# Optimization experiments

Measured on AMD Instinct MI355X. Metric: run time of the kernel, lower is better.

## Reference

```python
import jax, jax.numpy as jnp
import numpy as np

B, IN, H = 8192, 1024, 1024
WRANK, UR0, UR1, G = 256, 64, 32, 2
HG = H // G


def setup_inputs() -> dict:
    key = jax.random.key(0)
    ks = jax.random.split(key, 24)
    r = lambda k, shp: 0.1 * jax.random.normal(k, shp, dtype=jnp.float32)
    inp = {
        "x": jax.random.normal(ks[0], (B, IN), dtype=jnp.float32),
        "h": jax.random.normal(ks[1], (B, H), dtype=jnp.float32),
        "c": jax.random.normal(ks[2], (B, H), dtype=jnp.float32),
        "W": r(ks[3], (IN, WRANK)),
        "W1": r(ks[4], (WRANK, H)),
        "W2": r(ks[5], (WRANK, H)),
        "W3": r(ks[6], (WRANK, H)),
        "W4": r(ks[7], (WRANK, H)),
        "U": r(ks[8], (G, HG, UR0)),
        "U1": r(ks[9], (G, UR0, HG)),
        "U2": r(ks[10], (G, UR0, HG)),
        "U3": r(ks[11], (G, UR0, HG)),
        "U4": r(ks[12], (G, UR0, HG)),
        "UU": r(ks[13], (G, HG, UR1)),
        "UU1": r(ks[14], (G, UR1, HG)),
        "UU2": r(ks[15], (G, UR1, HG)),
        "UU3": r(ks[16], (G, UR1, HG)),
        "UU4": r(ks[17], (G, UR1, HG)),
        "bias_f": jnp.ones((1, H), dtype=jnp.float32),
        "bias_i": jnp.ones((1, H), dtype=jnp.float32),
        "bias_c": jnp.ones((1, H), dtype=jnp.float32),
        "bias_o": jnp.ones((1, H), dtype=jnp.float32),
    }
    return inp


def _grouped(hg, Ushare, Ui):
    # hg: [B, g, hg]; Ushare: [g, hg, r]; Ui: [g, r, hg] -> [B, H]
    t = jnp.einsum('bgd,gdr->bgr', hg, Ushare)
    return jnp.einsum('bgr,grd->bgd', t, Ui).reshape(hg.shape[0], H)


def reference(x, h, c, W, W1, W2, W3, W4, U, U1, U2, U3, U4,
              UU, UU1, UU2, UU3, UU4, bias_f, bias_i, bias_c, bias_o):
    # low-rank W path
    xw = x @ W                      # [B, wRank]
    wVal1, wVal2, wVal3, wVal4 = xw @ W1, xw @ W2, xw @ W3, xw @ W4

    # grouped low-rank U path (diagonal groups)
    hg = h.reshape(B, G, HG)
    tU = jnp.einsum('bgd,gdr->bgr', hg, U)          # shared projection
    uVal1 = jnp.einsum('bgr,grd->bgd', tU, U1).reshape(B, H)
    uVal2 = jnp.einsum('bgr,grd->bgd', tU, U2).reshape(B, H)
    uVal3 = jnp.einsum('bgr,grd->bgd', tU, U3).reshape(B, H)
    uVal4 = jnp.einsum('bgr,grd->bgd', tU, U4).reshape(B, H)

    # grouped UU path on group-rotated h (index = [1..g-1, 0])
    hg3 = jnp.roll(hg, -1, axis=1)
    tUU = jnp.einsum('bgd,gdr->bgr', hg3, UU)
    uuVal1 = jnp.einsum('bgr,grd->bgd', tUU, UU1).reshape(B, H)
    uuVal2 = jnp.einsum('bgr,grd->bgd', tUU, UU2).reshape(B, H)
    uuVal3 = jnp.einsum('bgr,grd->bgd', tUU, UU3).reshape(B, H)
    uuVal4 = jnp.einsum('bgr,grd->bgd', tUU, UU4).reshape(B, H)

    matVal_i = wVal1 + uVal1 + uuVal1
    matVal_f = wVal2 + uVal2 + uuVal2
    matVal_o = wVal3 + uVal3 + uuVal3
    matVal_c = wVal4 + uVal4 + uuVal4

    i = jax.nn.sigmoid(matVal_i + bias_i)
    f = jax.nn.sigmoid(matVal_f + bias_f)
    o = jax.nn.sigmoid(matVal_o + bias_o)
    c_tilda = jnp.tanh(matVal_c + bias_c)

    c_next = f * c + i * c_tilda
    h_next = o * jnp.tanh(c_next)
    return (c_next, h_next)
```

## Files before the change

### kernel.cpp

```cpp
#include <hip/hip_runtime.h>
#include <hip/hip_bf16.h>

#define B_ROWS 8192
#define IN_DIM 1024
#define H_DIM  1024
#define WRANK  256
#define UR0    64
#define UR1    32
#define HGD    512

#define NS2    11
#define NTA    14

typedef __attribute__((ext_vector_type(8))) short bf16x8;
typedef __attribute__((ext_vector_type(4))) float f32x4;
typedef __attribute__((ext_vector_type(4))) float float4v;

__device__ __forceinline__ unsigned short f2bf(float f) {
    union { float f; unsigned u; } v; v.f = f;
    unsigned r = v.u + 0x7FFF + ((v.u >> 16) & 1);
    return (unsigned short)(r >> 16);
}

__device__ __forceinline__ void gld16(void* lds, const void* g) {
    __builtin_amdgcn_global_load_lds(
        (const __attribute__((address_space(1))) unsigned int*)g,
        (__attribute__((address_space(3))) unsigned int*)lds, 16, 0, 0);
}

__device__ __forceinline__ float fsig(float x)  { return 1.f / (1.f + __expf(-x)); }
__device__ __forceinline__ float ftanh(float x) { return 1.f - 2.f / (__expf(2.f * x) + 1.f); }

__global__ __launch_bounds__(256)
void pack_weights(const float* __restrict__ W,
                  const float* __restrict__ W1, const float* __restrict__ W2,
                  const float* __restrict__ W3, const float* __restrict__ W4,
                  const float* __restrict__ U,  const float* __restrict__ U1,
                  const float* __restrict__ U2, const float* __restrict__ U3,
                  const float* __restrict__ U4,
                  const float* __restrict__ UU, const float* __restrict__ UU1,
                  const float* __restrict__ UU2,const float* __restrict__ UU3,
                  const float* __restrict__ UU4,
                  unsigned short* __restrict__ WbfT,
                  unsigned short* __restrict__ HPbf,
                  unsigned short* __restrict__ BT2)
{
    const float* Wg[4]  = {W1, W2, W3, W4};
    const float* Ug[4]  = {U1, U2, U3, U4};
    const float* UUg[4] = {UU1, UU2, UU3, UU4};
    const long N_WT = 256L * 1024;
    const long N_HP = 256L * 512;
    const long N_BT = 16L * NS2 * 8192;
    const long total = N_WT + N_HP + N_BT;
    for (long t = blockIdx.x * 256L + threadIdx.x; t < total; t += (long)gridDim.x * 256L) {
        if (t < N_WT) {
            int n = (int)(t >> 10), p = (int)(t & 1023);
            int span = p >> 6, slp = (p >> 3) & 7, e = p & 7;
            int k = span * 64 + ((slp ^ (n & 7)) << 3) + e;
            WbfT[t] = f2bf(W[(size_t)k * WRANK + n]);
        } else if (t < N_WT + N_HP) {
            long u = t - N_WT;
            int n = (int)(u >> 9), p = (int)(u & 511);
            int span = p >> 6, slp = (p >> 3) & 7, e = p & 7;
            int k = span * 64 + ((slp ^ (n & 7)) << 3) + e;
            float v;
            if (n < 64)       v = U [(size_t)k * UR0 + n];
            else if (n < 96)  v = UU[(size_t)(HGD + k) * UR1 + (n - 64)];
            else if (n < 128) v = 0.f;
            else if (n < 192) v = U [(size_t)(HGD + k) * UR0 + (n - 128)];
            else if (n < 224) v = UU[(size_t)k * UR1 + (n - 192)];
            else              v = 0.f;
            HPbf[u] = f2bf(v);
        } else {
            long u = t - N_WT - N_HP;
            int img = (int)(u >> 13);
            int nt = img / NS2, s = img % NS2;
            int r = (int)(u & 8191);
            int q = r >> 11, kc = (r >> 9) & 3, row = (r >> 3) & 63, e = r & 7;
            int n = nt * 64 + row, g = n >> 9, nn = n & 511;
            int kk = kc * 8 + e;
            float v;
            if (s < 8)       v = Wg[q][(size_t)(s * 32 + kk) * H_DIM + n];
            else if (s < 10) v = Ug[q][((size_t)g * UR0 + (s - 8) * 32 + kk) * HGD + nn];
            else             v = UUg[q][((size_t)g * UR1 + kk) * HGD + nn];
            BT2[u] = f2bf(v);
        }
    }
}

__global__ __launch_bounds__(256, 4)
void s1_kernel(const float* __restrict__ x, const float* __restrict__ h,
               const unsigned short* __restrict__ WbfT,
               const unsigned short* __restrict__ HPbf,
               unsigned short* __restrict__ A2T)
{
    __shared__ short As[64 * 64];
    __shared__ short Bs[2][64 * 64];

    const int flat = blockIdx.x;
    const int id = (flat & 7) * 128 + (flat >> 3);
    const int bx = id & 7, by = id >> 3;
    const int m0 = by * 64;

    const bool pa = bx < 4;
    const int Kdim = pa ? IN_DIM : HGD;
    const float* Af = pa ? x : h;
    const int a_off = pa ? 0 : ((bx - 4) >> 1) * HGD;
    const unsigned short* Bw = pa ? (WbfT + (size_t)(bx * 64) * IN_DIM)
                                  : (HPbf + (size_t)((bx - 4) * 64) * HGD);
    const int ldbw = pa ? IN_DIM : HGD;
    const int ccol0 = pa ? bx * 64 : WRANK + (bx - 4) * 64;

    const int tid = threadIdx.x, lane = tid & 63, wid = tid >> 6;
    const int wr = wid >> 1, wc = wid & 1;
    const int lr = lane & 15, lh = lane >> 4;
    const int l8 = lane >> 3, l7 = lane & 7;

    f32x4 acc[2][2];
    #pragma unroll
    for (int i = 0; i < 2; ++i)
        #pragma unroll
        for (int j = 0; j < 2; ++j) acc[i][j] = (f32x4){0.f, 0.f, 0.f, 0.f};

    float4v areg[2][2][2];

#define S1_STAGEB(buf, kk) do {                                                   \
    _Pragma("unroll")                                                             \
    for (int t = 0; t < 2; ++t) {                                                 \
        int u = wid * 2 + t;                                                      \
        gld16((char*)&Bs[buf][0] + u * 1024,                                      \
              (const char*)Bw + ((size_t)(u * 8 + l8) * ldbw + (kk)) * 2 + l7 * 16); \
    } } while (0)

#define S1_LOADA(set, kk) do {                                                    \
    _Pragma("unroll")                                                             \
    for (int t = 0; t < 2; ++t) {                                                 \
        int cc = tid + t * 256;                                                   \
        int row = cc >> 3, slot = cc & 7;                                         \
        const float* p = Af + (size_t)(m0 + row) * 1024 + a_off + (kk) + slot * 8;\
        areg[set][t][0] = *(const float4v*)p;                                     \
        areg[set][t][1] = *(const float4v*)(p + 4);                               \
    } } while (0)

#define S1_WRITEA(set) do {                                                       \
    _Pragma("unroll")                                                             \
    for (int t = 0; t < 2; ++t) {                                                 \
        int cc = tid + t * 256;                                                   \
        int row = cc >> 3, slot = cc & 7;                                         \
        union { bf16x8 v; unsigned short s_[8]; } uv;                             \
        uv.s_[0] = f2bf(areg[set][t][0].x); uv.s_[1] = f2bf(areg[set][t][0].y);   \
        uv.s_[2] = f2bf(areg[set][t][0].z); uv.s_[3] = f2bf(areg[set][t][0].w);   \
        uv.s_[4] = f2bf(areg[set][t][1].x); uv.s_[5] = f2bf(areg[set][t][1].y);   \
        uv.s_[6] = f2bf(areg[set][t][1].z); uv.s_[7] = f2bf(areg[set][t][1].w);   \
        *(bf16x8*)((char*)As + row * 128 + ((slot ^ (row & 7)) << 4)) = uv.v;     \
    } } while (0)

    S1_STAGEB(0, 0);
    S1_LOADA(0, 0);

    #pragma unroll
    for (int ki = 0; ki < 16; ++ki) {
        if (ki * 64 >= Kdim) break;
        const int cur = ki & 1;
        const bool more = (ki + 1) * 64 < Kdim;
        if (more) S1_STAGEB(cur ^ 1, (ki + 1) * 64);
        if (more) { asm volatile("s_waitcnt vmcnt(2)" ::: "memory"); }
        else      { asm volatile("s_waitcnt vmcnt(0)" ::: "memory"); }
        S1_WRITEA(cur);
        if (more) S1_LOADA(cur ^ 1, (ki + 1) * 64);
        asm volatile("s_waitcnt lgkmcnt(0)" ::: "memory");
        __builtin_amdgcn_s_barrier();
        asm volatile("" ::: "memory");
        #pragma unroll
        for (int ks = 0; ks < 2; ++ks) {
            bf16x8 af[2];
            #pragma unroll
            for (int i = 0; i < 2; ++i) {
                int r = wr * 32 + i * 16 + lr;
                af[i] = *(const bf16x8*)((const char*)As + r * 128
                        + (((ks * 4 + lh) ^ (r & 7)) << 4));
            }
            #pragma unroll
            for (int j = 0; j < 2; ++j) {
                int r = wc * 32 + j * 16 + lr;
                bf16x8 rb = *(const bf16x8*)((const char*)&Bs[cur][0] + r * 128
                            + (((ks * 4 + lh) ^ (r & 7)) << 4));
                #pragma unroll
                for (int i = 0; i < 2; ++i)
                    acc[i][j] = __builtin_amdgcn_mfma_f32_16x16x32_bf16(
                        af[i], rb, acc[i][j], 0, 0, 0);
            }
        }
        asm volatile("" ::: "memory");
        __builtin_amdgcn_s_barrier();
        asm volatile("" ::: "memory");
    }
#undef S1_STAGEB
#undef S1_LOADA
#undef S1_WRITEA

    #pragma unroll
    for (int i = 0; i < 2; ++i) {
        #pragma unroll
        for (int j = 0; j < 2; ++j) {
            int ncol = ccol0 + wc * 32 + j * 16 + lr;
            int blk = ncol >> 5;
            if (blk == 11 || blk == 15) continue;
            int tt = (blk <= 10) ? blk : blk - 1;
            int kk = ncol & 31, kc = kk >> 3, e = kk & 7;
            #pragma unroll
            for (int rr = 0; rr < 4; ++rr) {
                int brow = m0 + wr * 32 + i * 16 + lh * 4 + rr;
                A2T[((size_t)(brow >> 8) * NTA + tt) * 8192 + kc * 2048
                    + (brow & 255) * 8 + e] = f2bf(acc[i][j][rr]);
            }
        }
    }
}

__global__ __launch_bounds__(512, 4)
void s2_kernel(const unsigned short* __restrict__ A2T,
               const unsigned short* __restrict__ BT2,
               const float* __restrict__ bias_f, const float* __restrict__ bias_i,
               const float* __restrict__ bias_c, const float* __restrict__ bias_o,
               const float* __restrict__ cin,
               float* __restrict__ cout, float* __restrict__ hout)
{
    __shared__ short As[3][4 * 128 * 8];
    __shared__ short Bs[3][4 * 4 * 64 * 8];

    const int flat = blockIdx.x;
    const int id = (flat & 7) * 128 + (flat >> 3);
    const int nt = id & 15, mt = id >> 4;
    const int m0 = mt * 128, n0 = nt * 64, g = nt >> 3;

    const int tid = threadIdx.x, lane = tid & 63, wid = tid >> 6;
    const int wr = wid >> 2, wc = wid & 3;
    const int lr = lane & 15, lh = lane >> 4;

    const char* Abase = (const char*)A2T + (size_t)(mt >> 1) * NTA * 16384
                        + (wid >> 1) * 4096 + (mt & 1) * 2048 + (wid & 1) * 1024
                        + lane * 16;
    const char* Bbase = (const char*)BT2 + (size_t)nt * NS2 * 16384 + lane * 16;

    f32x4 acc[4][4];
    #pragma unroll
    for (int q = 0; q < 4; ++q)
        #pragma unroll
        for (int i = 0; i < 4; ++i) acc[q][i] = (f32x4){0.f, 0.f, 0.f, 0.f};

#define S2_TA(s) ((s) < 8 ? (s) : (g == 0 ? ((s) == 10 ? 13 : (s)) \
                                          : ((s) == 10 ? 10 : (s) + 3)))
#define S2_STAGE(buf, s, tA) do {                                                 \
    gld16((char*)&As[buf][0] + wid * 1024, Abase + (size_t)(tA) * 16384);         \
    _Pragma("unroll")                                                             \
    for (int t = 0; t < 2; ++t) {                                                 \
        int v = wid * 2 + t;                                                      \
        gld16((char*)&Bs[buf][0] + v * 1024,                                      \
              Bbase + (size_t)(s) * 16384 + v * 1024);                            \
    } } while (0)

    S2_STAGE(0, 0, 0);
    S2_STAGE(1, 1, 1);

    #pragma unroll
    for (int s = 0; s < NS2; ++s) {
        const int cur = s % 3;
        if (s + 2 < NS2) {
            S2_STAGE((s + 2) % 3, s + 2, S2_TA(s + 2));
            asm volatile("s_waitcnt vmcnt(6)" ::: "memory");
        } else if (s + 1 < NS2) {
            asm volatile("s_waitcnt vmcnt(3)" ::: "memory");
        } else {
            asm volatile("s_waitcnt vmcnt(0)" ::: "memory");
        }
        __builtin_amdgcn_s_barrier();
        asm volatile("" ::: "memory");

        bf16x8 rb[4];
        #pragma unroll
        for (int q = 0; q < 4; ++q)
            rb[q] = *(const bf16x8*)((const char*)&Bs[cur][0]
                    + q * 4096 + lh * 1024 + (wc * 16 + lr) * 16);
        {
            bf16x8 af0 = *(const bf16x8*)((const char*)&As[cur][0]
                         + lh * 2048 + (wr * 64 + 0 * 16 + lr) * 16);
            bf16x8 af1 = *(const bf16x8*)((const char*)&As[cur][0]
                         + lh * 2048 + (wr * 64 + 1 * 16 + lr) * 16);
            __builtin_amdgcn_s_setprio(1);
            #pragma unroll
            for (int q = 0; q < 4; ++q) {
                acc[q][0] = __builtin_amdgcn_mfma_f32_16x16x32_bf16(af0, rb[q], acc[q][0], 0, 0, 0);
                acc[q][1] = __builtin_amdgcn_mfma_f32_16x16x32_bf16(af1, rb[q], acc[q][1], 0, 0, 0);
            }
            __builtin_amdgcn_s_setprio(0);
        }
        asm volatile("" ::: "memory");
        __builtin_amdgcn_s_barrier();
        asm volatile("" ::: "memory");

        {
            bf16x8 af2 = *(const bf16x8*)((const char*)&As[cur][0]
                         + lh * 2048 + (wr * 64 + 2 * 16 + lr) * 16);
            bf16x8 af3 = *(const bf16x8*)((const char*)&As[cur][0]
                         + lh * 2048 + (wr * 64 + 3 * 16 + lr) * 16);
            __builtin_amdgcn_s_setprio(1);
            #pragma unroll
            for (int q = 0; q < 4; ++q) {
                acc[q][2] = __builtin_amdgcn_mfma_f32_16x16x32_bf16(af2, rb[q], acc[q][2], 0, 0, 0);
                acc[q][3] = __builtin_amdgcn_mfma_f32_16x16x32_bf16(af3, rb[q], acc[q][3], 0, 0, 0);
            }
            __builtin_amdgcn_s_setprio(0);
        }
        asm volatile("" ::: "memory");
        __builtin_amdgcn_s_barrier();
        asm volatile("" ::: "memory");
    }
#undef S2_STAGE
#undef S2_TA

    const int ncol = n0 + wc * 16 + lr;
    const float Bi = bias_i[ncol], Bf = bias_f[ncol];
    const float Bo = bias_o[ncol], Bc = bias_c[ncol];
    #pragma unroll
    for (int i = 0; i < 4; ++i) {
        #pragma unroll
        for (int rr = 0; rr < 4; ++rr) {
            int brow = m0 + wr * 64 + i * 16 + lh * 4 + rr;
            float mi = acc[0][i][rr] + Bi;
            float mf = acc[1][i][rr] + Bf;
            float mo = acc[2][i][rr] + Bo;
            float mc = acc[3][i][rr] + Bc;
            float iv = fsig(mi), fv = fsig(mf), ov = fsig(mo);
            float ct = ftanh(mc);
            float cv = cin[(size_t)brow * H_DIM + ncol];
            float cn = fv * cv + iv * ct;
            float hn = ov * ftanh(cn);
            cout[(size_t)brow * H_DIM + ncol] = cn;
            hout[(size_t)brow * H_DIM + ncol] = hn;
        }
    }
}

extern "C" void kernel_launch(void* const* d_in, const int* in_sizes, int n_in,
                              void* d_out, int out_size, void* d_ws, size_t ws_size,
                              hipStream_t stream)
{
    const float* x   = (const float*)d_in[0];
    const float* h   = (const float*)d_in[1];
    const float* c   = (const float*)d_in[2];
    const float* W   = (const float*)d_in[3];
    const float* W1  = (const float*)d_in[4];
    const float* W2  = (const float*)d_in[5];
    const float* W3  = (const float*)d_in[6];
    const float* W4  = (const float*)d_in[7];
    const float* U   = (const float*)d_in[8];
    const float* U1  = (const float*)d_in[9];
    const float* U2  = (const float*)d_in[10];
    const float* U3  = (const float*)d_in[11];
    const float* U4  = (const float*)d_in[12];
    const float* UU  = (const float*)d_in[13];
    const float* UU1 = (const float*)d_in[14];
    const float* UU2 = (const float*)d_in[15];
    const float* UU3 = (const float*)d_in[16];
    const float* UU4 = (const float*)d_in[17];
    const float* bias_f = (const float*)d_in[18];
    const float* bias_i = (const float*)d_in[19];
    const float* bias_c = (const float*)d_in[20];
    const float* bias_o = (const float*)d_in[21];

    unsigned short* A2T  = (unsigned short*)d_ws;
    unsigned short* WbfT = A2T  + 32L * NTA * 8192;
    unsigned short* HPbf = WbfT + 256L * 1024;
    unsigned short* BT2  = HPbf + 256L * 512;

    float* c_out = (float*)d_out;
    float* h_out = c_out + (size_t)B_ROWS * H_DIM;

    pack_weights<<<dim3(2048), dim3(256), 0, stream>>>(
        W, W1, W2, W3, W4, U, U1, U2, U3, U4, UU, UU1, UU2, UU3, UU4,
        WbfT, HPbf, BT2);

    s1_kernel<<<dim3(1024), dim3(256), 0, stream>>>(x, h, WbfT, HPbf, A2T);

    s2_kernel<<<dim3(1024), dim3(512), 0, stream>>>(
        A2T, BT2, bias_f, bias_i, bias_c, bias_o, c, c_out, h_out);
}
```

Baseline: 83.15 us.

## Move second-stage weight packing into extra s1 blocks to overlap with GEMM

The BT2 weight packing (W1-4, U1-4, UU1-4 to bf16 tiles) moves out of pack_weights and into 512 extra blocks appended to the s1 launch, so it runs concurrently with the first-stage GEMM. pack_weights now only packs the s1 operands with fewer blocks. This shortens the serial pre-pass but adds branch and argument overhead to s1, and the packing blocks compete with the GEMM for CUs and bandwidth.

```diff
diff --git a/kernel.cpp b/kernel.cpp
--- a/kernel.cpp
+++ b/kernel.cpp
@@ -33,32 +33,20 @@
 
 __global__ __launch_bounds__(256)
 void pack_weights(const float* __restrict__ W,
-                  const float* __restrict__ W1, const float* __restrict__ W2,
-                  const float* __restrict__ W3, const float* __restrict__ W4,
-                  const float* __restrict__ U,  const float* __restrict__ U1,
-                  const float* __restrict__ U2, const float* __restrict__ U3,
-                  const float* __restrict__ U4,
-                  const float* __restrict__ UU, const float* __restrict__ UU1,
-                  const float* __restrict__ UU2,const float* __restrict__ UU3,
-                  const float* __restrict__ UU4,
+                  const float* __restrict__ U,  const float* __restrict__ UU,
                   unsigned short* __restrict__ WbfT,
-                  unsigned short* __restrict__ HPbf,
-                  unsigned short* __restrict__ BT2)
+                  unsigned short* __restrict__ HPbf)
 {
-    const float* Wg[4]  = {W1, W2, W3, W4};
-    const float* Ug[4]  = {U1, U2, U3, U4};
-    const float* UUg[4] = {UU1, UU2, UU3, UU4};
     const long N_WT = 256L * 1024;
     const long N_HP = 256L * 512;
-    const long N_BT = 16L * NS2 * 8192;
-    const long total = N_WT + N_HP + N_BT;
+    const long total = N_WT + N_HP;
     for (long t = blockIdx.x * 256L + threadIdx.x; t < total; t += (long)gridDim.x * 256L) {
         if (t < N_WT) {
             int n = (int)(t >> 10), p = (int)(t & 1023);
             int span = p >> 6, slp = (p >> 3) & 7, e = p & 7;
             int k = span * 64 + ((slp ^ (n & 7)) << 3) + e;
             WbfT[t] = f2bf(W[(size_t)k * WRANK + n]);
-        } else if (t < N_WT + N_HP) {
+        } else {
             long u = t - N_WT;
             int n = (int)(u >> 9), p = (int)(u & 511);
             int span = p >> 6, slp = (p >> 3) & 7, e = p & 7;
@@ -71,8 +59,33 @@
             else if (n < 224) v = UU[(size_t)k * UR1 + (n - 192)];
             else              v = 0.f;
             HPbf[u] = f2bf(v);
-        } else {
-            long u = t - N_WT - N_HP;
+        }
+    }
+}
+
+__global__ __launch_bounds__(256, 4)
+void s1_kernel(const float* __restrict__ x, const float* __restrict__ h,
+               const unsigned short* __restrict__ WbfT,
+               const unsigned short* __restrict__ HPbf,
+               unsigned short* __restrict__ A2T,
+               unsigned short* __restrict__ BT2,
+               const float* __restrict__ W1, const float* __restrict__ W2,
+               const float* __restrict__ W3, const float* __restrict__ W4,
+               const float* __restrict__ U1, const float* __restrict__ U2,
+               const float* __restrict__ U3, const float* __restrict__ U4,
+               const float* __restrict__ UU1, const float* __restrict__ UU2,
+               const float* __restrict__ UU3, const float* __restrict__ UU4)
+{
+    __shared__ short As[64 * 64];
+    __shared__ short Bs[2][64 * 64];
+
+    if (blockIdx.x >= 1024) {
+        const float* Wg[4]  = {W1, W2, W3, W4};
+        const float* Ug[4]  = {U1, U2, U3, U4};
+        const float* UUg[4] = {UU1, UU2, UU3, UU4};
+        const long N_BT = 16L * NS2 * 8192;
+        for (long u = (blockIdx.x - 1024) * 256L + threadIdx.x; u < N_BT;
+             u += 512L * 256) {
             int img = (int)(u >> 13);
             int nt = img / NS2, s = img % NS2;
             int r = (int)(u & 8191);
@@ -85,17 +98,8 @@
             else             v = UUg[q][((size_t)g * UR1 + kk) * HGD + nn];
             BT2[u] = f2bf(v);
         }
-    }
-}
-
-__global__ __launch_bounds__(256, 4)
-void s1_kernel(const float* __restrict__ x, const float* __restrict__ h,
-               const unsigned short* __restrict__ WbfT,
-               const unsigned short* __restrict__ HPbf,
-               unsigned short* __restrict__ A2T)
-{
-    __shared__ short As[64 * 64];
-    __shared__ short Bs[2][64 * 64];
+        return;
+    }
 
     const int flat = blockIdx.x;
     const int id = (flat & 7) * 128 + (flat >> 3);
@@ -377,11 +381,11 @@
     float* c_out = (float*)d_out;
     float* h_out = c_out + (size_t)B_ROWS * H_DIM;
 
-    pack_weights<<<dim3(2048), dim3(256), 0, stream>>>(
-        W, W1, W2, W3, W4, U, U1, U2, U3, U4, UU, UU1, UU2, UU3, UU4,
-        WbfT, HPbf, BT2);
-
-    s1_kernel<<<dim3(1024), dim3(256), 0, stream>>>(x, h, WbfT, HPbf, A2T);
+    pack_weights<<<dim3(512), dim3(256), 0, stream>>>(W, U, UU, WbfT, HPbf);
+
+    s1_kernel<<<dim3(1536), dim3(256), 0, stream>>>(
+        x, h, WbfT, HPbf, A2T, BT2,
+        W1, W2, W3, W4, U1, U2, U3, U4, UU1, UU2, UU3, UU4);
 
     s2_kernel<<<dim3(1024), dim3(512), 0, stream>>>(
         A2T, BT2, bias_f, bias_i, bias_c, bias_o, c, c_out, h_out);
```

Result: faster. 79.66 us (median of 2 runs) (-4.2%).
